# Kernel optimization log

Measured on AMD Instinct MI355X. Metric: run time of the kernel, lower is better.

The kernel has to match this reference:

```python
import jax, jax.numpy as jnp
import numpy as np

B, D = 8192, 256
NUM_CLASSES = 128
CHUNK = 256          # matches module chunk_size; B % CHUNK == 0
TEMP = 0.07
EPS_NORM = 1e-12


def setup_inputs() -> dict:
    key = jax.random.key(0)
    k1, k2 = jax.random.split(key)
    features = jax.random.normal(k1, (B, D), dtype=jnp.float32)
    labels = jax.random.randint(k2, (B,), 0, NUM_CLASSES, dtype=jnp.int64)
    return {"features": features, "labels": labels}


def reference(features, labels):
    n = features.shape[0]
    temperature = max(TEMP, 1e-4)

    # F.normalize(dim=1): x / max(||x||, eps)
    norm = jnp.maximum(jnp.linalg.norm(features, axis=1, keepdims=True), EPS_NORM)
    f = features / norm
    # clamp is a no-op after normalization but kept for faithfulness
    f = jnp.clip(f, -1000.0, 1000.0)

    # [B, B] similarity; the torch loop computes exactly these rows chunk by chunk
    sim = jnp.matmul(f, f.T) / temperature

    # self-mask: each row i masks column i (diagonal of its chunk's square block)
    self_mask = ~jnp.eye(n, dtype=bool)

    # positive mask: same label, excluding self
    pos = (labels[:, None] == labels[None, :]) & self_mask
    # per-chunk fallback: if a 256-row chunk has no positives at all, use self_mask
    pos_c = pos.reshape(n // CHUNK, CHUNK, n)
    has_pos = pos_c.any(axis=(1, 2), keepdims=True)
    pos = jnp.where(has_pos, pos_c, self_mask.reshape(n // CHUNK, CHUNK, n)).reshape(n, n)

    # max-subtract BEFORE self-masking (faithful: includes self-sim = 1/temp)
    sim_max = jnp.max(sim, axis=1, keepdims=True)
    logits = jnp.clip(sim - jax.lax.stop_gradient(sim_max), -1000.0, 1000.0)

    exp_sim = jnp.maximum(jnp.exp(logits), 1e-8) * self_mask
    log_sum_exp = jnp.log(jnp.sum(exp_sim, axis=1, keepdims=True) + 1e-8)
    log_prob = jnp.maximum(logits - log_sum_exp, -1000.0)

    pos_pairs = jnp.sum(pos, axis=1)                      # [B] int
    row_loss = -jnp.sum(pos * log_prob, axis=1)           # [B]
    valid = pos_pairs > 0
    row_loss = jnp.where(valid, row_loss / jnp.maximum(pos_pairs, 1).astype(row_loss.dtype), 0.0)

    total_loss = jnp.sum(row_loss)
    total_pairs = jnp.sum(valid).astype(jnp.float32)
    mean_loss = total_loss / (total_pairs + 1e-8)
    loss = mean_loss  # reduction == 'mean'
    return loss, total_pairs, mean_loss
```

## Files before the change

kernel.cpp:

```cpp
#include <hip/hip_runtime.h>
#include <hip/hip_bf16.h>
#include <type_traits>

#define NB 8192
#define DD 256
#define INV_T (1.0f/0.07f)
#define NSPLIT 8
#define BM 256
#define BN 64
#define CPS (NB/NSPLIT)
#define NITER (CPS/BN)
#define BUFB (BN*DD*2)

typedef __attribute__((ext_vector_type(8))) short s8v;
typedef __attribute__((ext_vector_type(4))) float f4v;
typedef unsigned int u32;
typedef unsigned short u16;

#define OFF_FB   0
#define OFF_HIST (4*1024*1024)
#define OFF_SE   (OFF_HIST + 4096)
#define OFF_SP   (OFF_SE + NSPLIT*NB*4)
#define OFF_CL   (OFF_SP + NSPLIT*NB*4)
#define OFF_CV   (OFF_CL + 256)

__global__ void k_zero(int* __restrict__ hist) {
    hist[threadIdx.x] = 0;
}

__global__ void k_norm(const float* __restrict__ feat, const int* __restrict__ lab,
                       __hip_bfloat16* __restrict__ fb, int* __restrict__ hist) {
    const int t = threadIdx.x;
    const int w = t >> 6, l = t & 63;
    const int row = blockIdx.x * 4 + w;
    const float4 v = ((const float4*)feat)[row * 64 + l];
    float s = v.x * v.x + v.y * v.y + v.z * v.z + v.w * v.w;
    #pragma unroll
    for (int d = 32; d; d >>= 1) s += __shfl_xor(s, d, 64);
    const float scale = 1.0f / fmaxf(sqrtf(s), 1e-12f);
    __hip_bfloat16 h0 = __float2bfloat16(v.x * scale);
    __hip_bfloat16 h1 = __float2bfloat16(v.y * scale);
    __hip_bfloat16 h2 = __float2bfloat16(v.z * scale);
    __hip_bfloat16 h3 = __float2bfloat16(v.w * scale);
    ushort4 o;
    o.x = *(u16*)&h0; o.y = *(u16*)&h1; o.z = *(u16*)&h2; o.w = *(u16*)&h3;
    ((ushort4*)fb)[row * 64 + l] = o;
    if (l == 0) atomicAdd(&hist[lab[row]], 1);
}

__launch_bounds__(512, 2)
__global__ void k_main(const __hip_bfloat16* __restrict__ fb,
                       const int* __restrict__ lab,
                       float* __restrict__ SE, float* __restrict__ SP) {
    __shared__ __align__(16) char ldsB[2 * BUFB];
    __shared__ int ldsLab[CPS];
    const int tid = threadIdx.x;
    const int w = tid >> 6;
    const int l = tid & 63;
    const int l15 = l & 15, lg = l >> 4;
    const int bid = blockIdx.x;
    const int sp = bid & 7, rb = bid >> 3;
    const int wbase = rb * BM + w * 32;
    const int col0 = sp * CPS;

    ldsLab[tid]       = lab[col0 + tid];
    ldsLab[tid + 512] = lab[col0 + 512 + tid];

    s8v a[2][8];
    #pragma unroll
    for (int m = 0; m < 2; m++)
        #pragma unroll
        for (int kk = 0; kk < 8; kk++)
            a[m][kk] = *(const s8v*)(fb + (wbase + m * 16 + l15) * DD + kk * 32 + lg * 8);

    int labr[8];
    #pragma unroll
    for (int m = 0; m < 2; m++)
        #pragma unroll
        for (int r = 0; r < 4; r++)
            labr[m * 4 + r] = lab[wbase + m * 16 + lg * 4 + r];

    float sE[8], sPp[8];
    #pragma unroll
    for (int i = 0; i < 8; i++) { sE[i] = 0.f; sPp[i] = 0.f; }

    s8v st[4];
    auto load_tile = [&](int t) {
        const char* gsrc = (const char*)fb + (size_t)(col0 + t * BN) * (DD * 2);
        #pragma unroll
        for (int i = 0; i < 4; i++)
            st[i] = *(const s8v*)(gsrc + tid * 16 + i * 8192);
    };
    auto write_tile = [&](int bufoff) {
        #pragma unroll
        for (int i = 0; i < 4; i++) {
            const int x = tid * 16 + i * 8192;
            const int br = x >> 9, inrow = x & 511;
            *(s8v*)(ldsB + bufoff + (br * 512 | (inrow ^ ((br & 7) << 4)))) = st[i];
        }
    };

    auto run = [&](auto diagC) {
        constexpr bool DIAG = decltype(diagC)::value;
        load_tile(0);
        write_tile(0);
        __syncthreads();
        for (int t = 0; t < NITER; t++) {
            const int curoff = (t & 1) * BUFB;
            if (t + 1 < NITER) load_tile(t + 1);

            f4v acc[2][4];
            #pragma unroll
            for (int m = 0; m < 2; m++)
                #pragma unroll
                for (int n = 0; n < 4; n++)
                    acc[m][n] = (f4v){0.f, 0.f, 0.f, 0.f};

            #pragma unroll
            for (int kk = 0; kk < 8; kk++) {
                s8v bfr[4];
                #pragma unroll
                for (int n = 0; n < 4; n++) {
                    const int br = n * 16 + l15;
                    const int ad = (br * 512 + kk * 64 + lg * 16) ^ ((br & 7) << 4);
                    bfr[n] = *(const s8v*)(ldsB + curoff + ad);
                }
                #pragma unroll
                for (int m = 0; m < 2; m++)
                    #pragma unroll
                    for (int n = 0; n < 4; n++)
                        acc[m][n] = __builtin_amdgcn_mfma_f32_16x16x32_bf16(a[m][kk], bfr[n], acc[m][n], 0, 0, 0);
            }

            const int cb = col0 + t * BN;
            #pragma unroll
            for (int n = 0; n < 4; n++) {
                const int col = cb + n * 16 + l15;
                const int lc = ldsLab[t * BN + n * 16 + l15];
                #pragma unroll
                for (int m = 0; m < 2; m++)
                    #pragma unroll
                    for (int r = 0; r < 4; r++) {
                        const int idx = m * 4 + r;
                        const float logit = fmaf(acc[m][n][r], INV_T, -INV_T);
                        float e = fmaxf(__expf(logit), 1e-8f);
                        bool pos = (lc == labr[idx]);
                        if (DIAG) {
                            const int row = wbase + m * 16 + lg * 4 + r;
                            const bool nself = (row != col);
                            e = nself ? e : 0.f;
                            pos = pos && nself;
                        }
                        sE[idx] += e;
                        sPp[idx] += pos ? logit : 0.f;
                    }
            }

            if (t + 1 < NITER) write_tile(curoff ^ BUFB);
            __syncthreads();
        }
    };
    if ((rb >> 2) == sp) run(std::true_type{}); else run(std::false_type{});

    #pragma unroll
    for (int idx = 0; idx < 8; idx++) {
        #pragma unroll
        for (int d = 1; d < 16; d <<= 1) {
            sE[idx]  += __shfl_xor(sE[idx], d, 16);
            sPp[idx] += __shfl_xor(sPp[idx], d, 16);
        }
    }
    if (l15 == 0) {
        #pragma unroll
        for (int idx = 0; idx < 8; idx++) {
            const int row = wbase + (idx >> 2) * 16 + lg * 4 + (idx & 3);
            SE[sp * NB + row] = sE[idx];
            SP[sp * NB + row] = sPp[idx];
        }
    }
}

__global__ void k_rows(const int* __restrict__ lab, const int* __restrict__ hist,
                       const float* __restrict__ SE, const float* __restrict__ SP,
                       float* __restrict__ CL, float* __restrict__ CV) {
    const int t = threadIdx.x;
    const int row = blockIdx.x * 256 + t;
    float se = 0.f, sp_ = 0.f;
    #pragma unroll
    for (int s = 0; s < NSPLIT; s++) {
        se  += SE[s * NB + row];
        sp_ += SP[s * NB + row];
    }
    const int n = hist[lab[row]] - 1;
    const float lse = logf(se + 1e-8f);
    const bool valid = n > 0;
    float loss = valid ? (lse - sp_ / (float)n) : 0.f;
    float vf = valid ? 1.f : 0.f;
    #pragma unroll
    for (int d = 32; d; d >>= 1) { loss += __shfl_xor(loss, d, 64); vf += __shfl_xor(vf, d, 64); }
    __shared__ float pl[4], pv[4];
    if ((t & 63) == 0) { pl[t >> 6] = loss; pv[t >> 6] = vf; }
    __syncthreads();
    if (t == 0) {
        CL[blockIdx.x] = pl[0] + pl[1] + pl[2] + pl[3];
        CV[blockIdx.x] = pv[0] + pv[1] + pv[2] + pv[3];
    }
}

__global__ void k_final(const float* __restrict__ CL, const float* __restrict__ CV,
                        float* __restrict__ out) {
    const int t = threadIdx.x;
    float lsum = (t < 32) ? CL[t] : 0.f;
    float vsum = (t < 32) ? CV[t] : 0.f;
    #pragma unroll
    for (int d = 32; d; d >>= 1) { lsum += __shfl_xor(lsum, d, 64); vsum += __shfl_xor(vsum, d, 64); }
    if (t == 0) {
        const float mean = lsum / (vsum + 1e-8f);
        out[0] = mean;
        out[1] = vsum;
        out[2] = mean;
    }
}

extern "C" void kernel_launch(void* const* d_in, const int* in_sizes, int n_in,
                              void* d_out, int out_size, void* d_ws, size_t ws_size,
                              hipStream_t stream) {
    (void)in_sizes; (void)n_in; (void)out_size; (void)ws_size;
    const float* feat = (const float*)d_in[0];
    const int*   lab  = (const int*)d_in[1];
    char* ws = (char*)d_ws;
    __hip_bfloat16* fb = (__hip_bfloat16*)(ws + OFF_FB);
    int*   hist = (int*)(ws + OFF_HIST);
    float* SE = (float*)(ws + OFF_SE);
    float* SP = (float*)(ws + OFF_SP);
    float* CL = (float*)(ws + OFF_CL);
    float* CV = (float*)(ws + OFF_CV);
    float* out = (float*)d_out;

    hipLaunchKernelGGL(k_zero,  dim3(1), dim3(128), 0, stream, hist);
    hipLaunchKernelGGL(k_norm,  dim3(NB / 4), dim3(256), 0, stream, feat, lab, fb, hist);
    hipLaunchKernelGGL(k_main,  dim3(NB / BM * NSPLIT), dim3(512), 0, stream, fb, lab, SE, SP);
    hipLaunchKernelGGL(k_rows,  dim3(NB / 256), dim3(256), 0, stream, lab, hist, SE, SP, CL, CV);
    hipLaunchKernelGGL(k_final, dim3(1), dim3(64), 0, stream, CL, CV, out);
}
```

Before: 80.31 us.

## Cut launches, shrink row tile to 128, and use exp2 in main loop

Removes the zero and final kernels. The label histogram is now built in shared memory inside k_rows, and a last-block atomic counter does the final reduction there. k_main switches to 256-thread blocks with BM=128, giving 512 blocks with twice as many LDS tile loads per thread. The exponential is computed with exp2f on pre-scaled logits, and k_rows rescales by ln2. The risks are every k_rows block redundantly building the histogram from 8192 labels, and k_main doubling its global B-tile traffic per output row.

```diff
diff --git a/kernel.cpp b/kernel.cpp
--- a/kernel.cpp
+++ b/kernel.cpp
@@ -5,8 +5,11 @@
 #define NB 8192
 #define DD 256
 #define INV_T (1.0f/0.07f)
+#define LOG2E 1.4426950408889634f
+#define LN2   0.6931471805599453f
+#define K1    (INV_T*LOG2E)
 #define NSPLIT 8
-#define BM 256
+#define BM 128
 #define BN 64
 #define CPS (NB/NSPLIT)
 #define NITER (CPS/BN)
@@ -18,18 +21,15 @@
 typedef unsigned short u16;
 
 #define OFF_FB   0
-#define OFF_HIST (4*1024*1024)
-#define OFF_SE   (OFF_HIST + 4096)
+#define OFF_SE   (4*1024*1024)
 #define OFF_SP   (OFF_SE + NSPLIT*NB*4)
 #define OFF_CL   (OFF_SP + NSPLIT*NB*4)
 #define OFF_CV   (OFF_CL + 256)
-
-__global__ void k_zero(int* __restrict__ hist) {
-    hist[threadIdx.x] = 0;
-}
-
-__global__ void k_norm(const float* __restrict__ feat, const int* __restrict__ lab,
-                       __hip_bfloat16* __restrict__ fb, int* __restrict__ hist) {
+#define OFF_CNT  (OFF_CV + 256)
+
+__global__ void k_norm(const float* __restrict__ feat,
+                       __hip_bfloat16* __restrict__ fb, int* __restrict__ cnt) {
+    if (blockIdx.x == 0 && threadIdx.x == 0) *cnt = 0;
     const int t = threadIdx.x;
     const int w = t >> 6, l = t & 63;
     const int row = blockIdx.x * 4 + w;
@@ -45,26 +45,25 @@
     ushort4 o;
     o.x = *(u16*)&h0; o.y = *(u16*)&h1; o.z = *(u16*)&h2; o.w = *(u16*)&h3;
     ((ushort4*)fb)[row * 64 + l] = o;
-    if (l == 0) atomicAdd(&hist[lab[row]], 1);
-}
-
-__launch_bounds__(512, 2)
+}
+
+__launch_bounds__(256, 2)
 __global__ void k_main(const __hip_bfloat16* __restrict__ fb,
                        const int* __restrict__ lab,
                        float* __restrict__ SE, float* __restrict__ SP) {
     __shared__ __align__(16) char ldsB[2 * BUFB];
     __shared__ int ldsLab[CPS];
     const int tid = threadIdx.x;
-    const int w = tid >> 6;
     const int l = tid & 63;
     const int l15 = l & 15, lg = l >> 4;
     const int bid = blockIdx.x;
     const int sp = bid & 7, rb = bid >> 3;
-    const int wbase = rb * BM + w * 32;
+    const int wbase = rb * BM + (tid >> 6) * 32;
     const int col0 = sp * CPS;
 
-    ldsLab[tid]       = lab[col0 + tid];
-    ldsLab[tid + 512] = lab[col0 + 512 + tid];
+    #pragma unroll
+    for (int i = 0; i < 4; i++)
+        ldsLab[tid + i * 256] = lab[col0 + tid + i * 256];
 
     s8v a[2][8];
     #pragma unroll
@@ -84,17 +83,17 @@
     #pragma unroll
     for (int i = 0; i < 8; i++) { sE[i] = 0.f; sPp[i] = 0.f; }
 
-    s8v st[4];
+    s8v st[8];
     auto load_tile = [&](int t) {
         const char* gsrc = (const char*)fb + (size_t)(col0 + t * BN) * (DD * 2);
         #pragma unroll
-        for (int i = 0; i < 4; i++)
-            st[i] = *(const s8v*)(gsrc + tid * 16 + i * 8192);
+        for (int i = 0; i < 8; i++)
+            st[i] = *(const s8v*)(gsrc + tid * 16 + i * 4096);
     };
     auto write_tile = [&](int bufoff) {
         #pragma unroll
-        for (int i = 0; i < 4; i++) {
-            const int x = tid * 16 + i * 8192;
+        for (int i = 0; i < 8; i++) {
+            const int x = tid * 16 + i * 4096;
             const int br = x >> 9, inrow = x & 511;
             *(s8v*)(ldsB + bufoff + (br * 512 | (inrow ^ ((br & 7) << 4)))) = st[i];
         }
@@ -142,8 +141,8 @@
                     #pragma unroll
                     for (int r = 0; r < 4; r++) {
                         const int idx = m * 4 + r;
-                        const float logit = fmaf(acc[m][n][r], INV_T, -INV_T);
-                        float e = fmaxf(__expf(logit), 1e-8f);
+                        const float lg2 = fmaf(acc[m][n][r], K1, -K1);
+                        float e = fmaxf(exp2f(lg2), 1e-8f);
                         bool pos = (lc == labr[idx]);
                         if (DIAG) {
                             const int row = wbase + m * 16 + lg * 4 + r;
@@ -152,7 +151,7 @@
                             pos = pos && nself;
                         }
                         sE[idx] += e;
-                        sPp[idx] += pos ? logit : 0.f;
+                        sPp[idx] += pos ? lg2 : 0.f;
                     }
             }
 
@@ -160,7 +159,7 @@
             __syncthreads();
         }
     };
-    if ((rb >> 2) == sp) run(std::true_type{}); else run(std::false_type{});
+    if ((rb >> 3) == sp) run(std::true_type{}); else run(std::false_type{});
 
     #pragma unroll
     for (int idx = 0; idx < 8; idx++) {
@@ -180,10 +179,19 @@
     }
 }
 
-__global__ void k_rows(const int* __restrict__ lab, const int* __restrict__ hist,
+__global__ void k_rows(const int* __restrict__ lab,
                        const float* __restrict__ SE, const float* __restrict__ SP,
-                       float* __restrict__ CL, float* __restrict__ CV) {
+                       float* __restrict__ CL, float* __restrict__ CV,
+                       int* __restrict__ cnt, float* __restrict__ out) {
+    __shared__ int h[128];
     const int t = threadIdx.x;
+    if (t < 128) h[t] = 0;
+    __syncthreads();
+    #pragma unroll
+    for (int i = 0; i < 32; i++)
+        atomicAdd(&h[lab[t + i * 256]], 1);
+    __syncthreads();
+
     const int row = blockIdx.x * 256 + t;
     float se = 0.f, sp_ = 0.f;
     #pragma unroll
@@ -191,34 +199,36 @@
         se  += SE[s * NB + row];
         sp_ += SP[s * NB + row];
     }
-    const int n = hist[lab[row]] - 1;
+    const int n = h[lab[row]] - 1;
     const float lse = logf(se + 1e-8f);
     const bool valid = n > 0;
-    float loss = valid ? (lse - sp_ / (float)n) : 0.f;
+    float loss = valid ? (lse - sp_ * LN2 / (float)n) : 0.f;
     float vf = valid ? 1.f : 0.f;
     #pragma unroll
     for (int d = 32; d; d >>= 1) { loss += __shfl_xor(loss, d, 64); vf += __shfl_xor(vf, d, 64); }
     __shared__ float pl[4], pv[4];
+    __shared__ int isLast;
     if ((t & 63) == 0) { pl[t >> 6] = loss; pv[t >> 6] = vf; }
     __syncthreads();
     if (t == 0) {
         CL[blockIdx.x] = pl[0] + pl[1] + pl[2] + pl[3];
         CV[blockIdx.x] = pv[0] + pv[1] + pv[2] + pv[3];
-    }
-}
-
-__global__ void k_final(const float* __restrict__ CL, const float* __restrict__ CV,
-                        float* __restrict__ out) {
-    const int t = threadIdx.x;
-    float lsum = (t < 32) ? CL[t] : 0.f;
-    float vsum = (t < 32) ? CV[t] : 0.f;
-    #pragma unroll
-    for (int d = 32; d; d >>= 1) { lsum += __shfl_xor(lsum, d, 64); vsum += __shfl_xor(vsum, d, 64); }
-    if (t == 0) {
-        const float mean = lsum / (vsum + 1e-8f);
-        out[0] = mean;
-        out[1] = vsum;
-        out[2] = mean;
+        __threadfence();
+        isLast = (atomicAdd(cnt, 1) == 31);
+    }
+    __syncthreads();
+    if (isLast) {
+        __threadfence();
+        float lsum = (t < 32) ? CL[t] : 0.f;
+        float vsum = (t < 32) ? CV[t] : 0.f;
+        #pragma unroll
+        for (int d = 32; d; d >>= 1) { lsum += __shfl_xor(lsum, d, 64); vsum += __shfl_xor(vsum, d, 64); }
+        if (t == 0) {
+            const float mean = lsum / (vsum + 1e-8f);
+            out[0] = mean;
+            out[1] = vsum;
+            out[2] = mean;
+        }
     }
 }
 
@@ -230,16 +240,14 @@
     const int*   lab  = (const int*)d_in[1];
     char* ws = (char*)d_ws;
     __hip_bfloat16* fb = (__hip_bfloat16*)(ws + OFF_FB);
-    int*   hist = (int*)(ws + OFF_HIST);
     float* SE = (float*)(ws + OFF_SE);
     float* SP = (float*)(ws + OFF_SP);
     float* CL = (float*)(ws + OFF_CL);
     float* CV = (float*)(ws + OFF_CV);
+    int*   cnt = (int*)(ws + OFF_CNT);
     float* out = (float*)d_out;
 
-    hipLaunchKernelGGL(k_zero,  dim3(1), dim3(128), 0, stream, hist);
-    hipLaunchKernelGGL(k_norm,  dim3(NB / 4), dim3(256), 0, stream, feat, lab, fb, hist);
-    hipLaunchKernelGGL(k_main,  dim3(NB / BM * NSPLIT), dim3(512), 0, stream, fb, lab, SE, SP);
-    hipLaunchKernelGGL(k_rows,  dim3(NB / 256), dim3(256), 0, stream, lab, hist, SE, SP, CL, CV);
-    hipLaunchKernelGGL(k_final, dim3(1), dim3(64), 0, stream, CL, CV, out);
-}
+    hipLaunchKernelGGL(k_norm, dim3(NB / 4), dim3(256), 0, stream, feat, fb, cnt);
+    hipLaunchKernelGGL(k_main, dim3(NB / BM * NSPLIT), dim3(256), 0, stream, fb, lab, SE, SP);
+    hipLaunchKernelGGL(k_rows, dim3(NB / 256), dim3(256), 0, stream, lab, SE, SP, CL, CV, cnt, out);
+}
```

New measurement: 71.67 us. 10.8% less time.
